# Kernel optimization log

Hardware: AMD Instinct MI355X
Metric: run time of the kernel (lower is better)

## Reference

```python
import jax, jax.numpy as jnp
import numpy as np

NUM_HEADS = 12
HEAD_DIM = 64
SCALE = HEAD_DIM ** -0.5


def setup_inputs() -> dict:
    key = jax.random.key(0)
    k1, k2, k3, k4, k5 = jax.random.split(key, 5)
    B, N, C = 4, 2048, NUM_HEADS * HEAD_DIM
    x = jax.random.normal(k1, (B, N, C), dtype=jnp.float32)
    W_qkv = jax.random.normal(k2, (C, 3 * C), dtype=jnp.float32) * (C ** -0.5)
    b_qkv = jax.random.normal(k3, (3 * C,), dtype=jnp.float32) * 0.02
    W_proj = jax.random.normal(k4, (C, C), dtype=jnp.float32) * (C ** -0.5)
    b_proj = jax.random.normal(k5, (C,), dtype=jnp.float32) * 0.02
    return {"x": x, "W_qkv": W_qkv, "b_qkv": b_qkv, "W_proj": W_proj, "b_proj": b_proj}


def reference(x, W_qkv, b_qkv, W_proj, b_proj):
    B, N, C = x.shape
    H, D = NUM_HEADS, HEAD_DIM
    qkv = x @ W_qkv + b_qkv                      # [B, N, 3C]
    qkv = qkv.reshape(B, N, 3, H, D)
    q = qkv[:, :, 0].transpose(0, 2, 1, 3) * SCALE  # [B, H, N, D]
    k = qkv[:, :, 1].transpose(0, 2, 1, 3)          # [B, H, N, D]
    v = qkv[:, :, 2].transpose(0, 2, 1, 3)          # [B, H, N, D]
    attn = jnp.einsum("bhnd,bhmd->bhnm", q, k)   # [B, H, N, N]
    attn = jax.nn.softmax(attn, axis=-1)
    ctx = jnp.einsum("bhnm,bhmd->bhnd", attn, v)  # [B, H, N, D]
    attn_out = ctx.transpose(0, 2, 1, 3).reshape(B, N, C)
    out = attn_out @ W_proj + b_proj
    return (out, attn_out)
```

## Files before the change

### kernel.cpp

```cpp
#include <hip/hip_runtime.h>
#include <stdint.h>

typedef unsigned short u16;
using bf16x8 = __attribute__((ext_vector_type(8))) __bf16;
using s16x8  = __attribute__((ext_vector_type(8))) short;
using s16x4  = __attribute__((ext_vector_type(4))) short;
using f32x4  = __attribute__((ext_vector_type(4))) float;

#define SCALE_Q 0.125f
#define LOG2E 1.44269504088896f

__device__ __forceinline__ u16 f2bf(float f) {
  union { float f; uint32_t u; } v; v.f = f;
  uint32_t u = v.u;
  return (u16)((u + 0x7FFFu + ((u >> 16) & 1)) >> 16);
}

__device__ __forceinline__ bf16x8 ld_frag(const u16* p) {
  return __builtin_bit_cast(bf16x8, *(const s16x8*)p);
}

__device__ __forceinline__ f32x4 MF(bf16x8 a, bf16x8 b, f32x4 c) {
  return __builtin_amdgcn_mfma_f32_16x16x32_bf16(a, b, c, 0, 0, 0);
}
__device__ __forceinline__ f32x4 MF16(s16x4 a, s16x4 b, f32x4 c) {
  return __builtin_amdgcn_mfma_f32_16x16x16bf16_1k(a, b, c, 0, 0, 0);
}

__device__ __forceinline__ void gld16(const u16* g, u16* l) {
  __builtin_amdgcn_global_load_lds(
      (const __attribute__((address_space(1))) uint32_t*)g,
      (__attribute__((address_space(3))) uint32_t*)l, 16, 0, 0);
}

__device__ __forceinline__ uint32_t pk_bf16(float a, float b) {
  uint32_t u0 = __builtin_bit_cast(uint32_t, a) + 0x8000u;
  uint32_t u1 = __builtin_bit_cast(uint32_t, b) + 0x8000u;
  return __builtin_amdgcn_perm(u1, u0, 0x07060302u);
}

__global__ void cvt_f32_bf16(const float* __restrict__ in, u16* __restrict__ out, int n) {
  int i = (blockIdx.x * 256 + threadIdx.x) * 4;
  if (i < n) {
    float4 v = *(const float4*)(in + i);
    uint2 o;
    o.x = (uint32_t)f2bf(v.x) | ((uint32_t)f2bf(v.y) << 16);
    o.y = (uint32_t)f2bf(v.z) | ((uint32_t)f2bf(v.w) << 16);
    *(uint2*)(out + i) = o;
  }
}

__global__ void transpose_cvt(const float* __restrict__ in, u16* __restrict__ out, int R, int C) {
  __shared__ float tile[32][33];
  int c0 = blockIdx.x * 32, r0 = blockIdx.y * 32;
  int tx = threadIdx.x & 31, ty = threadIdx.x >> 5;
#pragma unroll
  for (int j = 0; j < 32; j += 8)
    tile[ty + j][tx] = in[(size_t)(r0 + ty + j) * C + c0 + tx];
  __syncthreads();
#pragma unroll
  for (int j = 0; j < 32; j += 8)
    out[(size_t)(c0 + ty + j) * R + r0 + tx] = f2bf(tile[tx][ty + j]);
}

__global__ __launch_bounds__(256) void gemm_qkv(
    const u16* __restrict__ A, const u16* __restrict__ Bt, const float* __restrict__ bias,
    u16* __restrict__ q_out, u16* __restrict__ k_out, u16* __restrict__ v_out) {
  constexpr int K = 768;
  __shared__ __align__(16) u16 smem[17408];
  u16* sA = smem;
  u16* sB = smem + 8192;
  const int tid = threadIdx.x;
  const int lane = tid & 63, wave = tid >> 6;
  const int ml = lane & 15, kg = lane >> 4;
  const int wr = wave >> 1, wc = wave & 1;
  const int bn = blockIdx.x, bm = blockIdx.y;

  f32x4 acc[4][4] = {};
  const u16* Abase = A + (size_t)(bm * 128) * K;
  const u16* Bbase = Bt + (size_t)(bn * 128) * K;

  for (int k0 = 0; k0 < K; k0 += 64) {
#pragma unroll
    for (int p = 0; p < 4; p++) {
      int q = p * 256 + tid;
      int r = q >> 3, s = q & 7, c = s ^ (r & 7);
      gld16(Abase + (size_t)r * K + k0 + c * 8, sA + q * 8);
      gld16(Bbase + (size_t)r * K + k0 + c * 8, sB + q * 8);
    }
    __syncthreads();
#pragma unroll
    for (int kc = 0; kc < 2; kc++) {
      bf16x8 af[4], bfr[4];
      int ac = kc * 4 + kg;
#pragma unroll
      for (int i = 0; i < 4; i++) {
        int arow = wr * 64 + i * 16 + ml;
        af[i] = ld_frag(sA + (arow * 8 + (ac ^ (arow & 7))) * 8);
        int brow = wc * 64 + i * 16 + ml;
        bfr[i] = ld_frag(sB + (brow * 8 + (ac ^ (brow & 7))) * 8);
      }
#pragma unroll
      for (int mi = 0; mi < 4; mi++)
#pragma unroll
        for (int ni = 0; ni < 4; ni++)
          acc[mi][ni] = MF(af[mi], bfr[ni], acc[mi][ni]);
    }
    __syncthreads();
  }

  if (bn >= 12) {
    uint32_t* t32 = (uint32_t*)smem;
#pragma unroll
    for (int ni = 0; ni < 4; ni++) {
      int n_local = wc * 64 + ni * 16 + ml;
      float bv = bias[bn * 128 + n_local];
#pragma unroll
      for (int mi = 0; mi < 4; mi++) {
        int mh = wr * 32 + mi * 8 + kg * 2;
        t32[n_local * 68 + mh]     = pk_bf16(acc[mi][ni][0] + bv, acc[mi][ni][1] + bv);
        t32[n_local * 68 + mh + 1] = pk_bf16(acc[mi][ni][2] + bv, acc[mi][ni][3] + bv);
      }
    }
    __syncthreads();
    int row = tid >> 1, seg = tid & 1;
    int dg = (bn - 12) * 128 + row;
    int h = dg >> 6, d = dg & 63;
    int bi = bm >> 4, tok0 = (bm & 15) * 128;
    u16* dst = v_out + ((size_t)(bi * 12 + h) * 64 + d) * 2048 + tok0 + seg * 64;
    const uint32_t* src = t32 + row * 68 + seg * 32;
#pragma unroll
    for (int j = 0; j < 8; j++)
      *(uint4*)(dst + j * 8) = *(const uint4*)(src + j * 4);
  } else {
#pragma unroll
    for (int ni = 0; ni < 4; ni++) {
      int n = bn * 128 + wc * 64 + ni * 16 + ml;
      int s = n >> 9 >= 1 ? (n >= 768 ? 1 : 0) : 0;
      int rem = n - s * 768;
      int h = rem >> 6, d = rem & 63;
      float bv = bias[n];
      u16* dst = (s == 0) ? q_out : k_out;
      float scl = (s == 0) ? SCALE_Q * LOG2E : 1.0f;
#pragma unroll
      for (int mi = 0; mi < 4; mi++) {
        int m0 = bm * 128 + wr * 64 + mi * 16 + kg * 4;
#pragma unroll
        for (int r = 0; r < 4; r++) {
          int m = m0 + r;
          int bi = m >> 11, tok = m & 2047;
          dst[(size_t)(bi * 12 + h) * 131072 + (size_t)tok * 64 + d] = f2bf((acc[mi][ni][r] + bv) * scl);
        }
      }
    }
  }
}

__global__ __launch_bounds__(256) void gemm_proj(
    const u16* __restrict__ A, const u16* __restrict__ Bt, const float* __restrict__ bias,
    float* __restrict__ c_out) {
  constexpr int K = 768;
  __shared__ __align__(16) u16 sA[128 * 64];
  __shared__ __align__(16) u16 sB[64 * 64];
  const int tid = threadIdx.x;
  const int lane = tid & 63, wave = tid >> 6;
  const int ml = lane & 15, kg = lane >> 4;
  const int bn = blockIdx.x, bm = blockIdx.y;
  f32x4 acc[2][4] = {};
  const u16* Abase = A + (size_t)(bm * 128) * K;
  const u16* Bbase = Bt + (size_t)(bn * 64) * K;

  for (int k0 = 0; k0 < K; k0 += 64) {
#pragma unroll
    for (int p = 0; p < 4; p++) {
      int q = p * 256 + tid;
      int r = q >> 3, s = q & 7, c = s ^ (r & 7);
      gld16(Abase + (size_t)r * K + k0 + c * 8, sA + q * 8);
    }
#pragma unroll
    for (int p = 0; p < 2; p++) {
      int q = p * 256 + tid;
      int r = q >> 3, s = q & 7, c = s ^ (r & 7);
      gld16(Bbase + (size_t)r * K + k0 + c * 8, sB + q * 8);
    }
    __syncthreads();
#pragma unroll
    for (int kc = 0; kc < 2; kc++) {
      int ac = kc * 4 + kg;
      bf16x8 af[2], bfr[4];
#pragma unroll
      for (int i = 0; i < 2; i++) {
        int arow = wave * 32 + i * 16 + ml;
        af[i] = ld_frag(sA + (arow * 8 + (ac ^ (arow & 7))) * 8);
      }
#pragma unroll
      for (int i = 0; i < 4; i++) {
        int brow = i * 16 + ml;
        bfr[i] = ld_frag(sB + (brow * 8 + (ac ^ (brow & 7))) * 8);
      }
#pragma unroll
      for (int mi = 0; mi < 2; mi++)
#pragma unroll
        for (int ni = 0; ni < 4; ni++)
          acc[mi][ni] = MF(af[mi], bfr[ni], acc[mi][ni]);
    }
    __syncthreads();
  }
#pragma unroll
  for (int ni = 0; ni < 4; ni++) {
    int n = bn * 64 + ni * 16 + ml;
    float bv = bias[n];
#pragma unroll
    for (int mi = 0; mi < 2; mi++) {
      int m0 = bm * 128 + wave * 32 + mi * 16 + kg * 4;
#pragma unroll
      for (int r = 0; r < 4; r++)
        c_out[(size_t)(m0 + r) * 768 + n] = acc[mi][ni][r] + bv;
    }
  }
}

__global__ __launch_bounds__(256, 3) void attn_kernel(
    const u16* __restrict__ qs, const u16* __restrict__ ks, const u16* __restrict__ vt,
    float* __restrict__ attn_f32, u16* __restrict__ attn_bf) {
  __shared__ __align__(16) u16 sK[2][64 * 64];
  __shared__ __align__(16) u16 sV[2][64 * 64];
  const int tid = threadIdx.x, lane = tid & 63, wave = tid >> 6;
  const int ml = lane & 15, kg = lane >> 4;
  const int bh = blockIdx.y;
  const int q0 = blockIdx.x * 128 + wave * 32;
  const size_t base = (size_t)bh * 2048 * 64;

  bf16x8 qf[2][2];
#pragma unroll
  for (int qt = 0; qt < 2; qt++) {
    const u16* qp = qs + base + (size_t)(q0 + qt * 16 + ml) * 64 + kg * 8;
    qf[qt][0] = ld_frag(qp);
    qf[qt][1] = ld_frag(qp + 32);
  }
  f32x4 l4[2] = {};
  f32x4 O[2][4] = {};

  int buf = 0;
  auto stage = [&](int b, int kt) {
#pragma unroll
    for (int p = 0; p < 2; p++) {
      int q = p * 256 + tid;
      int r = q >> 3, s = q & 7, c = s ^ (r & 7);
      gld16(ks + base + (size_t)(kt + r) * 64 + c * 8, &sK[b][q * 8]);
      gld16(vt + base + (size_t)r * 2048 + kt + c * 8, &sV[b][q * 8]);
    }
  };

  stage(0, 0);
  for (int kt = 0; kt < 2048; kt += 64) {
    __syncthreads();
    if (kt + 64 < 2048) stage(buf ^ 1, kt + 64);

    f32x4 sc[2][4] = {};
#pragma unroll
    for (int nt = 0; nt < 4; nt++) {
#pragma unroll
      for (int kc = 0; kc < 2; kc++) {
        int krow = nt * 16 + ml;
        int c = kc * 4 + kg;
        bf16x8 kf = ld_frag(&sK[buf][(krow * 8 + (c ^ (krow & 7))) * 8]);
        sc[0][nt] = MF(kf, qf[0][kc], sc[0][nt]);
        sc[1][nt] = MF(kf, qf[1][kc], sc[1][nt]);
      }
    }

    s16x4 pb[2][4];
#pragma unroll
    for (int qt = 0; qt < 2; qt++)
#pragma unroll
      for (int nt = 0; nt < 4; nt++) {
        f32x4 p;
#pragma unroll
        for (int r = 0; r < 4; r++) p[r] = __builtin_amdgcn_exp2f(sc[qt][nt][r]);
        l4[qt] += p;
        uint2 w;
        w.x = pk_bf16(p[0], p[1]);
        w.y = pk_bf16(p[2], p[3]);
        pb[qt][nt] = __builtin_bit_cast(s16x4, w);
      }

#pragma unroll
    for (int dt = 0; dt < 4; dt++) {
      int r = dt * 16 + ml;
#pragma unroll
      for (int kc4 = 0; kc4 < 4; kc4++) {
        int c0 = kc4 * 2 + (kg >> 1);
        s16x4 vf = *(const s16x4*)(&sV[buf][((r * 8 + (c0 ^ (r & 7))) * 8 + (kg & 1) * 4)]);
        O[0][dt] = MF16(vf, pb[0][kc4], O[0][dt]);
        O[1][dt] = MF16(vf, pb[1][kc4], O[1][dt]);
      }
    }
    buf ^= 1;
  }

  int b = bh / 12, h = bh - b * 12;
#pragma unroll
  for (int qt = 0; qt < 2; qt++) {
    float s = l4[qt][0] + l4[qt][1] + l4[qt][2] + l4[qt][3];
    s += __shfl_xor(s, 16);
    s += __shfl_xor(s, 32);
    float inv = __builtin_amdgcn_rcpf(s);
    int qrow = q0 + qt * 16 + ml;
    size_t rowoff = ((size_t)(b * 2048 + qrow)) * 768 + h * 64;
#pragma unroll
    for (int dt = 0; dt < 4; dt++) {
      f32x4 v = O[qt][dt];
      float4 o4 = {v[0] * inv, v[1] * inv, v[2] * inv, v[3] * inv};
      int d0 = dt * 16 + kg * 4;
      *(float4*)(attn_f32 + rowoff + d0) = o4;
      uint2 w;
      w.x = pk_bf16(o4.x, o4.y);
      w.y = pk_bf16(o4.z, o4.w);
      *(uint2*)(attn_bf + rowoff + d0) = w;
    }
  }
}

extern "C" void kernel_launch(void* const* d_in, const int* in_sizes, int n_in,
                              void* d_out, int out_size, void* d_ws, size_t ws_size,
                              hipStream_t stream) {
  const float* x      = (const float*)d_in[0];
  const float* W_qkv  = (const float*)d_in[1];
  const float* b_qkv  = (const float*)d_in[2];
  const float* W_proj = (const float*)d_in[3];
  const float* b_proj = (const float*)d_in[4];
  float* out      = (float*)d_out;
  float* attn_out = out + (size_t)8192 * 768;

  char* ws = (char*)d_ws;
  const size_t SZ_XB = (size_t)8192 * 768 * 2;
  u16* xb      = (u16*)(ws);
  u16* wqkv_t  = (u16*)(ws + SZ_XB);
  u16* wproj_t = (u16*)(ws + SZ_XB + 3538944);
  u16* qs      = (u16*)(ws + SZ_XB + 3538944 + 1179648);
  u16* ks      = (u16*)((char*)qs + SZ_XB);
  u16* vt      = (u16*)((char*)ks + SZ_XB);
  u16* ab      = xb;

  cvt_f32_bf16<<<6144, 256, 0, stream>>>(x, xb, 8192 * 768);
  transpose_cvt<<<dim3(2304 / 32, 768 / 32), 256, 0, stream>>>(W_qkv, wqkv_t, 768, 2304);
  transpose_cvt<<<dim3(768 / 32, 768 / 32), 256, 0, stream>>>(W_proj, wproj_t, 768, 768);
  gemm_qkv<<<dim3(18, 64), 256, 0, stream>>>(xb, wqkv_t, b_qkv, qs, ks, vt);
  attn_kernel<<<dim3(16, 48), 256, 0, stream>>>(qs, ks, vt, attn_out, ab);
  gemm_proj<<<dim3(12, 64), 256, 0, stream>>>(ab, wproj_t, b_proj, out);
}
```

Baseline: 236.5 us.

## Route P through LDS for 16x16x32 MFMA, fuse prep kernels, precompute attention addresses

The attention P·V stage now writes the bf16 probabilities into a per-wave LDS tile and reads them back as 8-wide fragments. This lets it use the 16x16x32 bf16 MFMA in place of the 16x16x16 variant. K/V staging addresses and the swizzled LDS read pointers are precomputed outside the loop, and the loop is unrolled by two tiles. The three preprocessing launches are merged into one kernel, and the Q/K selection in the QKV epilogue becomes a per-block branch. The extra LDS traffic and footprint, plus the scattered scalar output stores, are traded for fewer MFMA issues and less address arithmetic.

```diff
diff --git a/kernel.cpp b/kernel.cpp
--- a/kernel.cpp
+++ b/kernel.cpp
@@ -4,7 +4,6 @@
 typedef unsigned short u16;
 using bf16x8 = __attribute__((ext_vector_type(8))) __bf16;
 using s16x8  = __attribute__((ext_vector_type(8))) short;
-using s16x4  = __attribute__((ext_vector_type(4))) short;
 using f32x4  = __attribute__((ext_vector_type(4))) float;
 
 #define SCALE_Q 0.125f
@@ -23,9 +22,6 @@
 __device__ __forceinline__ f32x4 MF(bf16x8 a, bf16x8 b, f32x4 c) {
   return __builtin_amdgcn_mfma_f32_16x16x32_bf16(a, b, c, 0, 0, 0);
 }
-__device__ __forceinline__ f32x4 MF16(s16x4 a, s16x4 b, f32x4 c) {
-  return __builtin_amdgcn_mfma_f32_16x16x16bf16_1k(a, b, c, 0, 0, 0);
-}
 
 __device__ __forceinline__ void gld16(const u16* g, u16* l) {
   __builtin_amdgcn_global_load_lds(
@@ -39,20 +35,28 @@
   return __builtin_amdgcn_perm(u1, u0, 0x07060302u);
 }
 
-__global__ void cvt_f32_bf16(const float* __restrict__ in, u16* __restrict__ out, int n) {
-  int i = (blockIdx.x * 256 + threadIdx.x) * 4;
-  if (i < n) {
-    float4 v = *(const float4*)(in + i);
+__global__ void prep_kernel(const float* __restrict__ x, u16* __restrict__ xb,
+                            const float* __restrict__ Wq, u16* __restrict__ wqt,
+                            const float* __restrict__ Wp, u16* __restrict__ wpt) {
+  __shared__ float tile[32][33];
+  int bx = blockIdx.x;
+  if (bx < 6144) {
+    int i = (bx * 256 + threadIdx.x) * 4;
+    float4 v = *(const float4*)(x + i);
     uint2 o;
     o.x = (uint32_t)f2bf(v.x) | ((uint32_t)f2bf(v.y) << 16);
     o.y = (uint32_t)f2bf(v.z) | ((uint32_t)f2bf(v.w) << 16);
-    *(uint2*)(out + i) = o;
-  }
-}
-
-__global__ void transpose_cvt(const float* __restrict__ in, u16* __restrict__ out, int R, int C) {
-  __shared__ float tile[32][33];
-  int c0 = blockIdx.x * 32, r0 = blockIdx.y * 32;
+    *(uint2*)(xb + i) = o;
+    return;
+  }
+  bx -= 6144;
+  const float* in;
+  u16* out;
+  int C, cb, rb;
+  const int R = 768;
+  if (bx < 1728) { in = Wq; out = wqt; C = 2304; cb = bx % 72; rb = bx / 72; }
+  else { bx -= 1728; in = Wp; out = wpt; C = 768; cb = bx % 24; rb = bx / 24; }
+  int c0 = cb * 32, r0 = rb * 32;
   int tx = threadIdx.x & 31, ty = threadIdx.x >> 5;
 #pragma unroll
   for (int j = 0; j < 32; j += 8)
@@ -133,15 +137,14 @@
     for (int j = 0; j < 8; j++)
       *(uint4*)(dst + j * 8) = *(const uint4*)(src + j * 4);
   } else {
+    u16* dst = (bn < 6) ? q_out : k_out;
+    float scl = (bn < 6) ? SCALE_Q * LOG2E : 1.0f;
 #pragma unroll
     for (int ni = 0; ni < 4; ni++) {
       int n = bn * 128 + wc * 64 + ni * 16 + ml;
-      int s = n >> 9 >= 1 ? (n >= 768 ? 1 : 0) : 0;
-      int rem = n - s * 768;
+      int rem = (bn < 6) ? n : n - 768;
       int h = rem >> 6, d = rem & 63;
       float bv = bias[n];
-      u16* dst = (s == 0) ? q_out : k_out;
-      float scl = (s == 0) ? SCALE_Q * LOG2E : 1.0f;
 #pragma unroll
       for (int mi = 0; mi < 4; mi++) {
         int m0 = bm * 128 + wr * 64 + mi * 16 + kg * 4;
@@ -223,13 +226,14 @@
 __global__ __launch_bounds__(256, 3) void attn_kernel(
     const u16* __restrict__ qs, const u16* __restrict__ ks, const u16* __restrict__ vt,
     float* __restrict__ attn_f32, u16* __restrict__ attn_bf) {
-  __shared__ __align__(16) u16 sK[2][64 * 64];
-  __shared__ __align__(16) u16 sV[2][64 * 64];
+  __shared__ __align__(16) u16 sK[2][4096];
+  __shared__ __align__(16) u16 sV[2][4096];
+  __shared__ __align__(16) u16 sP[4][2304];
   const int tid = threadIdx.x, lane = tid & 63, wave = tid >> 6;
   const int ml = lane & 15, kg = lane >> 4;
   const int bh = blockIdx.y;
   const int q0 = blockIdx.x * 128 + wave * 32;
-  const size_t base = (size_t)bh * 2048 * 64;
+  const size_t base = (size_t)bh * 131072;
 
   bf16x8 qf[2][2];
 #pragma unroll
@@ -241,85 +245,100 @@
   f32x4 l4[2] = {};
   f32x4 O[2][4] = {};
 
-  int buf = 0;
+  const int m7 = ml & 7;
+  const u16* kbase[2] = { &sK[0][ml * 64 + ((0 + kg) ^ m7) * 8],
+                          &sK[0][ml * 64 + ((4 + kg) ^ m7) * 8] };
+  const u16* vbase[2] = { &sV[0][ml * 64 + ((0 + kg) ^ m7) * 8],
+                          &sV[0][ml * 64 + ((4 + kg) ^ m7) * 8] };
+  u16* pw = &sP[wave][ml * 72 + kg * 4];
+  const u16* pr = &sP[wave][ml * 72 + kg * 8];
+
+  const int r0 = tid >> 3,          c0 = (tid & 7) ^ (r0 & 7);
+  const int r1 = (256 + tid) >> 3,  c1 = (tid & 7) ^ (r1 & 7);
+  const u16* kgp0 = ks + base + r0 * 64 + c0 * 8;
+  const u16* kgp1 = ks + base + r1 * 64 + c1 * 8;
+  const u16* vgp0 = vt + base + r0 * 2048 + c0 * 8;
+  const u16* vgp1 = vt + base + r1 * 2048 + c1 * 8;
+
   auto stage = [&](int b, int kt) {
-#pragma unroll
-    for (int p = 0; p < 2; p++) {
-      int q = p * 256 + tid;
-      int r = q >> 3, s = q & 7, c = s ^ (r & 7);
-      gld16(ks + base + (size_t)(kt + r) * 64 + c * 8, &sK[b][q * 8]);
-      gld16(vt + base + (size_t)r * 2048 + kt + c * 8, &sV[b][q * 8]);
-    }
+    gld16(kgp0 + kt * 64, &sK[b][tid * 8]);
+    gld16(kgp1 + kt * 64, &sK[b][2048 + tid * 8]);
+    gld16(vgp0 + kt,      &sV[b][tid * 8]);
+    gld16(vgp1 + kt,      &sV[b][2048 + tid * 8]);
   };
 
   stage(0, 0);
-  for (int kt = 0; kt < 2048; kt += 64) {
-    __syncthreads();
-    if (kt + 64 < 2048) stage(buf ^ 1, kt + 64);
-
-    f32x4 sc[2][4] = {};
-#pragma unroll
-    for (int nt = 0; nt < 4; nt++) {
+  for (int kt = 0; kt < 2048; kt += 128) {
+#pragma unroll
+    for (int half = 0; half < 2; half++) {
+      const int cur = kt + half * 64;
+      __syncthreads();
+      if (cur + 64 < 2048) stage(half ^ 1, cur + 64);
+
+      f32x4 sc[2][4] = {};
+#pragma unroll
+      for (int nt = 0; nt < 4; nt++)
+#pragma unroll
+        for (int kc = 0; kc < 2; kc++) {
+          bf16x8 kf = ld_frag(kbase[kc] + nt * 1024 + half * 4096);
+          sc[0][nt] = MF(kf, qf[0][kc], sc[0][nt]);
+          sc[1][nt] = MF(kf, qf[1][kc], sc[1][nt]);
+        }
+
+#pragma unroll
+      for (int qt = 0; qt < 2; qt++)
+#pragma unroll
+        for (int nt = 0; nt < 4; nt++) {
+          f32x4 p;
+#pragma unroll
+          for (int r = 0; r < 4; r++) p[r] = __builtin_amdgcn_exp2f(sc[qt][nt][r]);
+          l4[qt] += p;
+          uint2 w;
+          w.x = pk_bf16(p[0], p[1]);
+          w.y = pk_bf16(p[2], p[3]);
+          *(uint2*)(pw + qt * 1152 + nt * 16) = w;
+        }
+
+      asm volatile("s_waitcnt lgkmcnt(0)" ::: "memory");
+
 #pragma unroll
       for (int kc = 0; kc < 2; kc++) {
-        int krow = nt * 16 + ml;
-        int c = kc * 4 + kg;
-        bf16x8 kf = ld_frag(&sK[buf][(krow * 8 + (c ^ (krow & 7))) * 8]);
-        sc[0][nt] = MF(kf, qf[0][kc], sc[0][nt]);
-        sc[1][nt] = MF(kf, qf[1][kc], sc[1][nt]);
-      }
-    }
-
-    s16x4 pb[2][4];
-#pragma unroll
-    for (int qt = 0; qt < 2; qt++)
-#pragma unroll
-      for (int nt = 0; nt < 4; nt++) {
-        f32x4 p;
-#pragma unroll
-        for (int r = 0; r < 4; r++) p[r] = __builtin_amdgcn_exp2f(sc[qt][nt][r]);
-        l4[qt] += p;
-        uint2 w;
-        w.x = pk_bf16(p[0], p[1]);
-        w.y = pk_bf16(p[2], p[3]);
-        pb[qt][nt] = __builtin_bit_cast(s16x4, w);
-      }
-
-#pragma unroll
-    for (int dt = 0; dt < 4; dt++) {
-      int r = dt * 16 + ml;
-#pragma unroll
-      for (int kc4 = 0; kc4 < 4; kc4++) {
-        int c0 = kc4 * 2 + (kg >> 1);
-        s16x4 vf = *(const s16x4*)(&sV[buf][((r * 8 + (c0 ^ (r & 7))) * 8 + (kg & 1) * 4)]);
-        O[0][dt] = MF16(vf, pb[0][kc4], O[0][dt]);
-        O[1][dt] = MF16(vf, pb[1][kc4], O[1][dt]);
-      }
-    }
-    buf ^= 1;
-  }
-
-  int b = bh / 12, h = bh - b * 12;
+        bf16x8 pf0 = ld_frag(pr + kc * 32);
+        bf16x8 pf1 = ld_frag(pr + 1152 + kc * 32);
+#pragma unroll
+        for (int nt2 = 0; nt2 < 4; nt2++) {
+          bf16x8 vf = ld_frag(vbase[kc] + nt2 * 1024 + half * 4096);
+          O[0][nt2] = MF(pf0, vf, O[0][nt2]);
+          O[1][nt2] = MF(pf1, vf, O[1][nt2]);
+        }
+      }
+    }
+  }
+
+  float linv[2];
 #pragma unroll
   for (int qt = 0; qt < 2; qt++) {
     float s = l4[qt][0] + l4[qt][1] + l4[qt][2] + l4[qt][3];
     s += __shfl_xor(s, 16);
     s += __shfl_xor(s, 32);
-    float inv = __builtin_amdgcn_rcpf(s);
-    int qrow = q0 + qt * 16 + ml;
-    size_t rowoff = ((size_t)(b * 2048 + qrow)) * 768 + h * 64;
-#pragma unroll
-    for (int dt = 0; dt < 4; dt++) {
-      f32x4 v = O[qt][dt];
-      float4 o4 = {v[0] * inv, v[1] * inv, v[2] * inv, v[3] * inv};
-      int d0 = dt * 16 + kg * 4;
-      *(float4*)(attn_f32 + rowoff + d0) = o4;
-      uint2 w;
-      w.x = pk_bf16(o4.x, o4.y);
-      w.y = pk_bf16(o4.z, o4.w);
-      *(uint2*)(attn_bf + rowoff + d0) = w;
-    }
-  }
+    linv[qt] = __builtin_amdgcn_rcpf(s);
+  }
+  int b = bh / 12, h = bh - b * 12;
+#pragma unroll
+  for (int qt = 0; qt < 2; qt++)
+#pragma unroll
+    for (int r = 0; r < 4; r++) {
+      float inv = __shfl(linv[qt], kg * 4 + r, 64);
+      int qrow = q0 + qt * 16 + kg * 4 + r;
+      size_t rowoff = ((size_t)(b * 2048 + qrow)) * 768 + h * 64;
+#pragma unroll
+      for (int nt2 = 0; nt2 < 4; nt2++) {
+        float v = O[qt][nt2][r] * inv;
+        int d = nt2 * 16 + ml;
+        attn_f32[rowoff + d] = v;
+        attn_bf[rowoff + d] = f2bf(v);
+      }
+    }
 }
 
 extern "C" void kernel_launch(void* const* d_in, const int* in_sizes, int n_in,
@@ -343,9 +362,7 @@
   u16* vt      = (u16*)((char*)ks + SZ_XB);
   u16* ab      = xb;
 
-  cvt_f32_bf16<<<6144, 256, 0, stream>>>(x, xb, 8192 * 768);
-  transpose_cvt<<<dim3(2304 / 32, 768 / 32), 256, 0, stream>>>(W_qkv, wqkv_t, 768, 2304);
-  transpose_cvt<<<dim3(768 / 32, 768 / 32), 256, 0, stream>>>(W_proj, wproj_t, 768, 768);
+  prep_kernel<<<6144 + 1728 + 576, 256, 0, stream>>>(x, xb, W_qkv, wqkv_t, W_proj, wproj_t);
   gemm_qkv<<<dim3(18, 64), 256, 0, stream>>>(xb, wqkv_t, b_qkv, qs, ks, vt);
   attn_kernel<<<dim3(16, 48), 256, 0, stream>>>(qs, ks, vt, attn_out, ab);
   gemm_proj<<<dim3(12, 64), 256, 0, stream>>>(ab, wproj_t, b_proj, out);
```

Measured after the change: 228.1 us. 1.04x faster.
